# Performance work log

Hardware: AMD Instinct MI355X
Metric: run time of the kernel (lower is better)

## Reference

```python
import jax, jax.numpy as jnp
import numpy as np

LN_EPS = 1e-5

def setup_inputs() -> dict:
    key = jax.random.key(0)
    B, S, D = 4, 2048, 1024
    ks = jax.random.split(key, 8)
    sc = 1.0 / np.sqrt(D)
    inp = {
        'x': jax.random.normal(ks[0], (B, S, D), jnp.float32),
        'Wq': jax.random.normal(ks[1], (D, D), jnp.float32) * sc,
        'bq': jnp.zeros((D,), jnp.float32),
        'Wk': jax.random.normal(ks[2], (D, D), jnp.float32) * sc,
        'bk': jnp.zeros((D,), jnp.float32),
        'Wv': jax.random.normal(ks[3], (D, D), jnp.float32) * sc,
        'bv': jnp.zeros((D,), jnp.float32),
        'Wo': jax.random.normal(ks[4], (D, D), jnp.float32) * sc,
        'bo': jnp.zeros((D,), jnp.float32),
        'Wg_val': jax.random.normal(ks[5], (D, D), jnp.float32) * sc,
        'bg_val': jnp.zeros((D,), jnp.float32),
        'Wg_gate': jax.random.normal(ks[6], (D, D), jnp.float32) * sc,
        'bg_gate': jnp.zeros((D,), jnp.float32),
        'gamma': jnp.ones((D,), jnp.float32),
        'beta': jnp.zeros((D,), jnp.float32),
    }
    return inp


def reference(x, Wq, bq, Wk, bk, Wv, bv, Wo, bo, Wg_val, bg_val, Wg_gate, bg_gate, gamma, beta):
    # x: [B,S,D]
    q = jnp.einsum('bsd,de->bse', x, Wq) + bq
    k = jnp.einsum('bsd,de->bse', x, Wk) + bk
    v = jnp.einsum('bsd,de->bse', x, Wv) + bv
    scale = 1.0 / jnp.sqrt(jnp.asarray(q.shape[-1], q.dtype))
    qk = jnp.einsum('bqe,bke->bqk', q, k) * scale  # [B,S,S]
    a = jax.nn.softmax(qk, axis=-1)
    out = jnp.einsum('bqk,bke->bqe', a, v)
    out = jnp.einsum('bse,ed->bsd', out, Wo) + bo
    # GLU residual on q, then LayerNorm
    glu = (jnp.einsum('bse,ed->bsd', q, Wg_val) + bg_val) * jax.nn.sigmoid(jnp.einsum('bse,ed->bsd', q, Wg_gate) + bg_gate)
    out = out + glu
    mu = jnp.mean(out, axis=-1, keepdims=True)
    var = jnp.var(out, axis=-1, keepdims=True)
    out = (out - mu) * jax.lax.rsqrt(var + LN_EPS) * gamma + beta
    return out
```

## Files before the change

### kernel.cpp

```cpp
#include <hip/hip_runtime.h>
#include <hip/hip_bf16.h>
#include <cstdint>


typedef __bf16 bf16x8 __attribute__((ext_vector_type(8)));
typedef __bf16 bf16x4 __attribute__((ext_vector_type(4)));
typedef float f32x4 __attribute__((ext_vector_type(4)));

#define SYNC() do { asm volatile("" ::: "memory"); __builtin_amdgcn_s_barrier(); asm volatile("" ::: "memory"); } while (0)
#define WAITV(n) asm volatile("s_waitcnt vmcnt(" #n ")" ::: "memory")

__device__ __forceinline__ void gload_lds16(const void* g, void* l) {
    __builtin_amdgcn_global_load_lds(
        (__attribute__((address_space(1))) void*)(uintptr_t)g,
        (__attribute__((address_space(3))) void*)(uintptr_t)l,
        16, 0, 0);
}

__device__ __forceinline__ float to_f32(float x) { return x; }
__device__ __forceinline__ float to_f32(__hip_bfloat16 x) { return __bfloat162float(x); }

template <int EPI, bool VTS>
__global__ __launch_bounds__(512, 1) void gemm256(
    const __hip_bfloat16* __restrict__ A1, int lda1,
    const __hip_bfloat16* __restrict__ A2, int lda2, int nsplit,
    const __hip_bfloat16* __restrict__ Bt,
    __hip_bfloat16* __restrict__ Cout, const float* __restrict__ bias, float scale,
    __hip_bfloat16* __restrict__ vt, int vtc0,
    int K, int ldb, int ldc,
    long strideA, long strideB, long strideC)
{
    __shared__ __align__(16) char smem[131072];

    const int b = blockIdx.z;
    const int tid = threadIdx.x;
    const int lane = tid & 63;
    const int wm = (tid >> 6) & 1;
    const int wn = (tid >> 6) >> 1;

    const bool sel2 = ((int)blockIdx.y * 256) >= nsplit;
    const __hip_bfloat16* A = sel2 ? A2 : A1;
    const int lda = sel2 ? lda2 : lda1;

    const __hip_bfloat16* gA = A + (long)b * strideA + (long)blockIdx.x * 256 * lda;
    const __hip_bfloat16* gB = Bt + (long)b * strideB + (long)blockIdx.y * 256 * ldb;

    const int r0 = tid >> 3;
    const int s0 = (tid & 7) ^ (r0 & 7);
    const int r1 = r0 + 64;
    const int s1 = (tid & 7) ^ (r1 & 7);

#define STAGE(buf, isB, half, kt)                                                        \
    do {                                                                                 \
        const __hip_bfloat16* g_ = (isB) ? gB : gA;                                      \
        const int ld_ = (isB) ? ldb : lda;                                               \
        char* l_ = smem + (buf) * 65536 + (isB) * 32768 + (half) * 16384;                \
        gload_lds16(g_ + (long)((half) * 128 + r0) * ld_ + (kt) * 64 + s0 * 8, l_ + tid * 16);        \
        gload_lds16(g_ + (long)((half) * 128 + r1) * ld_ + (kt) * 64 + s1 * 8, l_ + 8192 + tid * 16); \
    } while (0)

    const int fr = lane & 15;
    const int kg = lane >> 4;

#define LDA_(dst, buf, mh, mi, kk)                                                       \
    do {                                                                                 \
        const int lr_ = wm * 64 + (mi) * 16 + fr;                                        \
        const int sl_ = ((kk) * 4 + kg) ^ (lr_ & 7);                                     \
        dst = *(const bf16x8*)(smem + (buf) * 65536 + (mh) * 16384 + lr_ * 128 + sl_ * 16); \
    } while (0)
#define LDB_(dst, buf, nh, ni, kk)                                                       \
    do {                                                                                 \
        const int lr_ = wn * 32 + (ni) * 16 + fr;                                        \
        const int sl_ = ((kk) * 4 + kg) ^ (lr_ & 7);                                     \
        dst = *(const bf16x8*)(smem + (buf) * 65536 + 32768 + (nh) * 16384 + lr_ * 128 + sl_ * 16); \
    } while (0)

    f32x4 acc[2][2][4][2];
#pragma unroll
    for (int mh = 0; mh < 2; ++mh)
#pragma unroll
        for (int nh = 0; nh < 2; ++nh)
#pragma unroll
            for (int mi = 0; mi < 4; ++mi)
#pragma unroll
                for (int ni = 0; ni < 2; ++ni) acc[mh][nh][mi][ni] = {0.f, 0.f, 0.f, 0.f};

    bf16x8 av[4][2], bv[2][2];

#define MFMA_QUAD(mh, nh)                                                                \
    do {                                                                                 \
        __builtin_amdgcn_s_setprio(1);                                                   \
        _Pragma("unroll")                                                                \
        for (int mi = 0; mi < 4; ++mi)                                                   \
            _Pragma("unroll")                                                            \
            for (int ni = 0; ni < 2; ++ni)                                               \
                _Pragma("unroll")                                                        \
                for (int kk = 0; kk < 2; ++kk)                                           \
                    acc[mh][nh][mi][ni] = __builtin_amdgcn_mfma_f32_16x16x32_bf16(       \
                        av[mi][kk], bv[ni][kk], acc[mh][nh][mi][ni], 0, 0, 0);           \
        __builtin_amdgcn_s_setprio(0);                                                   \
    } while (0)

    const int NT = K >> 6;

    STAGE(0, 0, 0, 0);
    STAGE(0, 1, 0, 0);
    STAGE(0, 1, 1, 0);
    STAGE(0, 0, 1, 0);
    WAITV(4);
    SYNC();

    for (int t = 0; t < NT - 1; ++t) {
        const int c = t & 1;
#pragma unroll
        for (int mi = 0; mi < 4; ++mi) { LDA_(av[mi][0], c, 0, mi, 0); LDA_(av[mi][1], c, 0, mi, 1); }
#pragma unroll
        for (int ni = 0; ni < 2; ++ni) { LDB_(bv[ni][0], c, 0, ni, 0); LDB_(bv[ni][1], c, 0, ni, 1); }
        STAGE(c ^ 1, 0, 0, t + 1);
        MFMA_QUAD(0, 0);
        WAITV(4);
        SYNC();
#pragma unroll
        for (int ni = 0; ni < 2; ++ni) { LDB_(bv[ni][0], c, 1, ni, 0); LDB_(bv[ni][1], c, 1, ni, 1); }
        STAGE(c ^ 1, 1, 0, t + 1);
        MFMA_QUAD(0, 1);
        WAITV(4);
        SYNC();
#pragma unroll
        for (int mi = 0; mi < 4; ++mi) { LDA_(av[mi][0], c, 1, mi, 0); LDA_(av[mi][1], c, 1, mi, 1); }
        STAGE(c ^ 1, 1, 1, t + 1);
        MFMA_QUAD(1, 1);
        SYNC();
#pragma unroll
        for (int ni = 0; ni < 2; ++ni) { LDB_(bv[ni][0], c, 0, ni, 0); LDB_(bv[ni][1], c, 0, ni, 1); }
        STAGE(c ^ 1, 0, 1, t + 1);
        MFMA_QUAD(1, 0);
        WAITV(4);
        SYNC();
    }

    {
        const int c = (NT - 1) & 1;
#pragma unroll
        for (int mi = 0; mi < 4; ++mi) { LDA_(av[mi][0], c, 0, mi, 0); LDA_(av[mi][1], c, 0, mi, 1); }
#pragma unroll
        for (int ni = 0; ni < 2; ++ni) { LDB_(bv[ni][0], c, 0, ni, 0); LDB_(bv[ni][1], c, 0, ni, 1); }
        MFMA_QUAD(0, 0);
        WAITV(2);
        SYNC();
#pragma unroll
        for (int ni = 0; ni < 2; ++ni) { LDB_(bv[ni][0], c, 1, ni, 0); LDB_(bv[ni][1], c, 1, ni, 1); }
        MFMA_QUAD(0, 1);
        WAITV(0);
        SYNC();
#pragma unroll
        for (int mi = 0; mi < 4; ++mi) { LDA_(av[mi][0], c, 1, mi, 0); LDA_(av[mi][1], c, 1, mi, 1); }
        MFMA_QUAD(1, 1);
#pragma unroll
        for (int ni = 0; ni < 2; ++ni) { LDB_(bv[ni][0], c, 0, ni, 0); LDB_(bv[ni][1], c, 0, ni, 1); }
        MFMA_QUAD(1, 0);
    }

    const long row0 = (long)blockIdx.x * 256 + wm * 64 + (lane >> 4) * 4;
    const long col0 = (long)blockIdx.y * 256 + wn * 32 + (lane & 15);
#pragma unroll
    for (int mh = 0; mh < 2; ++mh) {
#pragma unroll
        for (int nh = 0; nh < 2; ++nh) {
#pragma unroll
            for (int ni = 0; ni < 2; ++ni) {
                const long col = col0 + nh * 128 + ni * 16;
                const float bval = (EPI == 0 && bias != nullptr) ? bias[col] : 0.f;
#pragma unroll
                for (int mi = 0; mi < 4; ++mi) {
                    const long row = row0 + mh * 128 + mi * 16;
                    if (VTS && col >= vtc0) {
                        const int b_ = (int)(row >> 11);
                        const int s_ = (int)(row & 2047);
                        bf16x4 pk;
#pragma unroll
                        for (int i = 0; i < 4; ++i) pk[i] = (__bf16)(acc[mh][nh][mi][ni][i] + bval);
                        *(bf16x4*)(vt + ((long)b_ << 21) + (long)(col - vtc0) * 2048 + s_) = pk;
                    } else {
#pragma unroll
                        for (int i = 0; i < 4; ++i) {
                            const float v = (EPI == 1) ? acc[mh][nh][mi][ni][i] * scale
                                                       : acc[mh][nh][mi][ni][i] + bval;
                            Cout[(long)b * strideC + (row + i) * (long)ldc + col] = __float2bfloat16(v);
                        }
                    }
                }
            }
        }
    }
#undef STAGE
#undef LDA_
#undef LDB_
#undef MFMA_QUAD
}

__global__ __launch_bounds__(512, 1) void gemm_tn128(
    const __hip_bfloat16* __restrict__ A, int lda,
    const __hip_bfloat16* __restrict__ Bt,
    __hip_bfloat16* __restrict__ Cout, const float* __restrict__ bias,
    int K, int ldb, int ldc,
    long strideA, long strideB, long strideC)
{
    __shared__ __align__(16) char smem[147456];

    const int b = blockIdx.z;
    const int tid = threadIdx.x;
    const int lane = tid & 63;
    const int wid = tid >> 6;
    const int wm = wid & 3;
    const int wn = wid >> 2;

    const __hip_bfloat16* gA = A + (long)b * strideA + (long)blockIdx.x * 256 * lda;
    const __hip_bfloat16* gB = Bt + (long)b * strideB + (long)blockIdx.y * 128 * ldb;

    const int r0 = tid >> 3, r1 = r0 + 64;
    const int s0 = (tid & 7) ^ (r0 & 7);
    const int s1 = (tid & 7) ^ (r1 & 7);

#define STG_A(base_, h_, kt_)                                                                              \
    do {                                                                                                   \
        gload_lds16(gA + (long)((h_) * 128 + r0) * lda + (kt_) * 64 + s0 * 8, (base_) + (h_) * 16384 + tid * 16);        \
        gload_lds16(gA + (long)((h_) * 128 + r1) * lda + (kt_) * 64 + s1 * 8, (base_) + (h_) * 16384 + 8192 + tid * 16); \
    } while (0)
#define STG_B(base_, kt_)                                                                                  \
    do {                                                                                                   \
        gload_lds16(gB + (long)r0 * ldb + (kt_) * 64 + s0 * 8, (base_) + 32768 + tid * 16);                \
        gload_lds16(gB + (long)r1 * ldb + (kt_) * 64 + s1 * 8, (base_) + 32768 + 8192 + tid * 16);         \
    } while (0)

    const int fr = lane & 15;
    const int kg = lane >> 4;

#define LD_A(dst, base_, mi_, kk_)                                                        \
    do {                                                                                  \
        const int row_ = wm * 64 + (mi_) * 16 + fr;                                       \
        const int sl_ = ((kk_) * 4 + kg) ^ (row_ & 7);                                    \
        dst = *(const bf16x8*)((base_) + row_ * 128 + sl_ * 16);                          \
    } while (0)
#define LD_B(dst, base_, ni_, kk_)                                                        \
    do {                                                                                  \
        const int row_ = wn * 64 + (ni_) * 16 + fr;                                       \
        const int sl_ = ((kk_) * 4 + kg) ^ (row_ & 7);                                    \
        dst = *(const bf16x8*)((base_) + 32768 + row_ * 128 + sl_ * 16);                  \
    } while (0)

    f32x4 acc[4][4];
#pragma unroll
    for (int mi = 0; mi < 4; ++mi)
#pragma unroll
        for (int ni = 0; ni < 4; ++ni) acc[mi][ni] = {0.f, 0.f, 0.f, 0.f};

    const int NT = K >> 6;

    STG_A(smem, 0, 0); STG_A(smem, 1, 0); STG_B(smem, 0);
    STG_A(smem + 49152, 0, 1); STG_A(smem + 49152, 1, 1); STG_B(smem + 49152, 1);
    WAITV(6);
    SYNC();

    int bi = 0;
    for (int t = 0; t < NT; ++t) {
        char* base = smem + bi * 49152;
        if (t + 2 < NT) {
            int bs = bi + 2; if (bs >= 3) bs -= 3;
            char* sb = smem + bs * 49152;
            STG_A(sb, 0, t + 2); STG_A(sb, 1, t + 2); STG_B(sb, t + 2);
        }
        bf16x8 av[4], bv[4];
#pragma unroll
        for (int kk = 0; kk < 2; ++kk) {
#pragma unroll
            for (int mi = 0; mi < 4; ++mi) LD_A(av[mi], base, mi, kk);
#pragma unroll
            for (int ni = 0; ni < 4; ++ni) LD_B(bv[ni], base, ni, kk);
            __builtin_amdgcn_s_setprio(1);
#pragma unroll
            for (int mi = 0; mi < 4; ++mi)
#pragma unroll
                for (int ni = 0; ni < 4; ++ni)
                    acc[mi][ni] = __builtin_amdgcn_mfma_f32_16x16x32_bf16(av[mi], bv[ni], acc[mi][ni], 0, 0, 0);
            __builtin_amdgcn_s_setprio(0);
        }
        if (t + 2 < NT) { WAITV(6); SYNC(); }
        else if (t + 1 < NT) { WAITV(0); SYNC(); }
        bi = (bi + 1 == 3) ? 0 : bi + 1;
    }

    const long row0 = (long)blockIdx.x * 256 + wm * 64 + (lane >> 4) * 4;
    const long col0 = (long)blockIdx.y * 128 + wn * 64 + (lane & 15);
#pragma unroll
    for (int ni = 0; ni < 4; ++ni) {
        const long col = col0 + ni * 16;
        const float bval = (bias != nullptr) ? bias[col] : 0.f;
#pragma unroll
        for (int mi = 0; mi < 4; ++mi) {
#pragma unroll
            for (int i = 0; i < 4; ++i) {
                const long row = row0 + mi * 16 + i;
                Cout[(long)b * strideC + row * (long)ldc + col] = __float2bfloat16(acc[mi][ni][i] + bval);
            }
        }
    }
#undef STG_A
#undef STG_B
#undef LD_A
#undef LD_B
}

__global__ __launch_bounds__(256) void transpose6(
    const float* __restrict__ W0, const float* __restrict__ W1, const float* __restrict__ W2,
    const float* __restrict__ W3, const float* __restrict__ W4, const float* __restrict__ W5,
    __hip_bfloat16* __restrict__ dst)
{
    __shared__ float tile[32][33];
    const int z = blockIdx.z;
    const float* pin = (z == 0) ? W0 : (z == 1) ? W1 : (z == 2) ? W2 : (z == 3) ? W3 : (z == 4) ? W4 : W5;
    __hip_bfloat16* pout = dst + (long)z * 1024 * 1024;
    const int tx = threadIdx.x, ty = threadIdx.y;
    const int c0 = blockIdx.x * 32, r0 = blockIdx.y * 32;
#pragma unroll
    for (int j = 0; j < 4; ++j)
        tile[ty + j * 8][tx] = pin[(long)(r0 + ty + j * 8) * 1024 + c0 + tx];
    __syncthreads();
#pragma unroll
    for (int j = 0; j < 4; ++j)
        pout[(long)(c0 + ty + j * 8) * 1024 + r0 + tx] = __float2bfloat16(tile[tx][ty + j * 8]);
}

__global__ __launch_bounds__(256) void f32_to_bf16_vec(
    const float* __restrict__ in, __hip_bfloat16* __restrict__ out, long n4)
{
    const long i = (long)blockIdx.x * 256 + threadIdx.x;
    if (i >= n4) return;
    const float4 v = ((const float4*)in)[i];
    union { __hip_bfloat16 h[4]; ushort4 u; } cv;
    cv.h[0] = __float2bfloat16(v.x);
    cv.h[1] = __float2bfloat16(v.y);
    cv.h[2] = __float2bfloat16(v.z);
    cv.h[3] = __float2bfloat16(v.w);
    ((ushort4*)out)[i] = cv.u;
}

__global__ __launch_bounds__(256) void concat_bias(
    const float* __restrict__ bq, const float* __restrict__ bk, const float* __restrict__ bv,
    const float* __restrict__ bo, const float* __restrict__ bgv, const float* __restrict__ bgg,
    float* __restrict__ out)
{
    const int i = blockIdx.x * 256 + threadIdx.x;
    float v;
    if (i < 1024) v = bq[i];
    else if (i < 2048) v = bk[i - 1024];
    else if (i < 3072) v = bv[i - 2048];
    else if (i < 4096) v = bo[i - 3072];
    else if (i < 5120) v = bgv[i - 4096];
    else v = bgg[i - 5120];
    out[i] = v;
}

__global__ __launch_bounds__(256) void softmax_kernel(
    const __hip_bfloat16* __restrict__ S, __hip_bfloat16* __restrict__ P)
{
    const long row = blockIdx.x;
    const __hip_bfloat16* s = S + row * 2048;
    __hip_bfloat16* p = P + row * 2048;
    const int t = threadIdx.x;
    const bf16x8 v8 = *(const bf16x8*)(s + t * 8);
    float v[8];
    float mx = -1e30f;
#pragma unroll
    for (int j = 0; j < 8; ++j) { v[j] = (float)v8[j]; mx = fmaxf(mx, v[j]); }
#pragma unroll
    for (int off = 32; off; off >>= 1) mx = fmaxf(mx, __shfl_xor(mx, off));
    __shared__ float wred[4];
    __shared__ float wsum[4];
    const int w = t >> 6;
    if ((t & 63) == 0) wred[w] = mx;
    __syncthreads();
    mx = fmaxf(fmaxf(wred[0], wred[1]), fmaxf(wred[2], wred[3]));
    float sum = 0.f;
#pragma unroll
    for (int j = 0; j < 8; ++j) { v[j] = __expf(v[j] - mx); sum += v[j]; }
#pragma unroll
    for (int off = 32; off; off >>= 1) sum += __shfl_xor(sum, off);
    if ((t & 63) == 0) wsum[w] = sum;
    __syncthreads();
    sum = wsum[0] + wsum[1] + wsum[2] + wsum[3];
    const float inv = 1.0f / sum;
    bf16x8 o8;
#pragma unroll
    for (int j = 0; j < 8; ++j) o8[j] = (__bf16)(v[j] * inv);
    *(bf16x8*)(p + t * 8) = o8;
}

__global__ __launch_bounds__(256) void glu_ln_kernel(
    const __hip_bfloat16* __restrict__ T1G,
    const float* __restrict__ gamma, const float* __restrict__ beta, float* __restrict__ out)
{
    const long row = blockIdx.x;
    const __hip_bfloat16* pr = T1G + row * 3072;
    const int t = threadIdx.x;
    const int c0 = t * 4;
    const bf16x4 t1 = *(const bf16x4*)(pr + c0);
    const bf16x4 gv = *(const bf16x4*)(pr + 1024 + c0);
    const bf16x4 gg = *(const bf16x4*)(pr + 2048 + c0);
    float y[4];
    float s = 0.f, ss = 0.f;
#pragma unroll
    for (int j = 0; j < 4; ++j) {
        const float g = (float)gv[j] * (1.0f / (1.0f + __expf(-(float)gg[j])));
        const float val = (float)t1[j] + g;
        y[j] = val; s += val; ss += val * val;
    }
#pragma unroll
    for (int off = 32; off; off >>= 1) { s += __shfl_xor(s, off); ss += __shfl_xor(ss, off); }
    __shared__ float rs[4], rss[4];
    const int w = t >> 6;
    if ((t & 63) == 0) { rs[w] = s; rss[w] = ss; }
    __syncthreads();
    s = rs[0] + rs[1] + rs[2] + rs[3];
    ss = rss[0] + rss[1] + rss[2] + rss[3];
    const float mu = s * (1.0f / 1024.0f);
    const float var = ss * (1.0f / 1024.0f) - mu * mu;
    const float r = rsqrtf(var + 1e-5f);
    const float4 gm = *(const float4*)(gamma + c0);
    const float4 bt = *(const float4*)(beta + c0);
    float4 o;
    o.x = (y[0] - mu) * r * gm.x + bt.x;
    o.y = (y[1] - mu) * r * gm.y + bt.y;
    o.z = (y[2] - mu) * r * gm.z + bt.z;
    o.w = (y[3] - mu) * r * gm.w + bt.w;
    *(float4*)(out + row * 1024 + c0) = o;
}

extern "C" void kernel_launch(void* const* d_in, const int* in_sizes, int n_in,
                              void* d_out, int out_size, void* d_ws, size_t ws_size,
                              hipStream_t stream)
{
    const int B = 4, S = 2048, D = 1024;
    const float* x    = (const float*)d_in[0];
    const float* Wq   = (const float*)d_in[1];
    const float* bq   = (const float*)d_in[2];
    const float* Wk   = (const float*)d_in[3];
    const float* bk   = (const float*)d_in[4];
    const float* Wv   = (const float*)d_in[5];
    const float* bv   = (const float*)d_in[6];
    const float* Wo   = (const float*)d_in[7];
    const float* bo   = (const float*)d_in[8];
    const float* Wgv  = (const float*)d_in[9];
    const float* bgv  = (const float*)d_in[10];
    const float* Wgg  = (const float*)d_in[11];
    const float* bgg  = (const float*)d_in[12];
    const float* gamma = (const float*)d_in[13];
    const float* beta  = (const float*)d_in[14];
    float* out = (float*)d_out;

    char* ws = (char*)d_ws;
    size_t off = 0;
    auto take = [&](size_t bytes) { char* p = ws + off; off += (bytes + 255) & ~(size_t)255; return p; };

    __hip_bfloat16* wcat   = (__hip_bfloat16*)take((size_t)6 * D * D * 2);
    float*          bcat   = (float*)take((size_t)6 * D * 4);
    __hip_bfloat16* xb     = (__hip_bfloat16*)take((size_t)B * S * D * 2);
    __hip_bfloat16* QKVb   = (__hip_bfloat16*)take((size_t)B * S * 3 * D * 2);
    __hip_bfloat16* Vtb    = (__hip_bfloat16*)take((size_t)B * S * D * 2);
    __hip_bfloat16* scoresb = (__hip_bfloat16*)take((size_t)B * S * S * 2);
    __hip_bfloat16* Pb     = (__hip_bfloat16*)take((size_t)B * S * S * 2);
    __hip_bfloat16* Oatt   = (__hip_bfloat16*)take((size_t)B * S * D * 2);
    __hip_bfloat16* T1G    = (__hip_bfloat16*)take((size_t)B * S * 3 * D * 2);

    const long SD = (long)S * D, SS = (long)S * S, S3D = (long)S * 3 * D;
    const float att_scale = 0.03125f;
    const __hip_bfloat16* Qb = QKVb;
    const __hip_bfloat16* Kb = QKVb + D;

    f32_to_bf16_vec<<<dim3((unsigned)((long)B * S * D / 4 / 256)), dim3(256), 0, stream>>>(x, xb, (long)B * S * D / 4);
    transpose6<<<dim3(D / 32, D / 32, 6), dim3(32, 8), 0, stream>>>(Wq, Wk, Wv, Wo, Wgv, Wgg, wcat);
    concat_bias<<<dim3(24), dim3(256), 0, stream>>>(bq, bk, bv, bo, bgv, bgg, bcat);

    gemm256<0, true><<<dim3(B * S / 256, 3 * D / 256, 1), dim3(512), 0, stream>>>(
        xb, D, xb, D, 1 << 30, wcat, QKVb, bcat, 1.f, Vtb, 2 * D,
        D, D, 3 * D, 0, 0, 0);

    gemm256<1, false><<<dim3(S / 256, S / 256, B), dim3(512), 0, stream>>>(
        Qb, 3 * D, Qb, 3 * D, 1 << 30, Kb, scoresb, nullptr, att_scale, nullptr, 1 << 30,
        D, 3 * D, S, S3D, S3D, SS);

    softmax_kernel<<<dim3(B * S), dim3(256), 0, stream>>>(scoresb, Pb);

    gemm_tn128<<<dim3(S / 256, D / 128, B), dim3(512), 0, stream>>>(
        Pb, S, Vtb, Oatt, nullptr, S, S, D, SS, SD, SD);

    gemm256<0, false><<<dim3(B * S / 256, 3 * D / 256, 1), dim3(512), 0, stream>>>(
        Oatt, D, QKVb, 3 * D, D, wcat + (size_t)3 * D * D, T1G, bcat + 3 * D, 1.f, nullptr, 1 << 30,
        D, D, 3 * D, 0, 0, 0);

    glu_ln_kernel<<<dim3(B * S), dim3(256), 0, stream>>>(T1G, gamma, beta, out);
}
```

Baseline: 244.6 us.

## Split fused QKV and output GEMMs into separate QK and V/gate launches

The fused QKV projection is split in two: a 256x256 GEMM writes Q and K, and a separate 128-wide-tile GEMM writes V directly in transposed layout. The final fused output GEMM is also split, with the gate projection moved to the 128-wide kernel. This shrinks the grid of the 256-tile kernels, presumably to fix wave quantization across the CUs and to take the transposed-store branch out of the big GEMM's epilogue. The cost is two extra kernel launches and re-reading xb and Q in separate passes.

```diff
diff --git a/kernel.cpp b/kernel.cpp
--- a/kernel.cpp
+++ b/kernel.cpp
@@ -17,16 +17,12 @@
         16, 0, 0);
 }
 
-__device__ __forceinline__ float to_f32(float x) { return x; }
-__device__ __forceinline__ float to_f32(__hip_bfloat16 x) { return __bfloat162float(x); }
-
-template <int EPI, bool VTS>
+template <int EPI>
 __global__ __launch_bounds__(512, 1) void gemm256(
     const __hip_bfloat16* __restrict__ A1, int lda1,
     const __hip_bfloat16* __restrict__ A2, int lda2, int nsplit,
     const __hip_bfloat16* __restrict__ Bt,
     __hip_bfloat16* __restrict__ Cout, const float* __restrict__ bias, float scale,
-    __hip_bfloat16* __restrict__ vt, int vtc0,
     int K, int ldb, int ldc,
     long strideA, long strideB, long strideC)
 {
@@ -174,20 +170,11 @@
 #pragma unroll
                 for (int mi = 0; mi < 4; ++mi) {
                     const long row = row0 + mh * 128 + mi * 16;
-                    if (VTS && col >= vtc0) {
-                        const int b_ = (int)(row >> 11);
-                        const int s_ = (int)(row & 2047);
-                        bf16x4 pk;
-#pragma unroll
-                        for (int i = 0; i < 4; ++i) pk[i] = (__bf16)(acc[mh][nh][mi][ni][i] + bval);
-                        *(bf16x4*)(vt + ((long)b_ << 21) + (long)(col - vtc0) * 2048 + s_) = pk;
-                    } else {
-#pragma unroll
-                        for (int i = 0; i < 4; ++i) {
-                            const float v = (EPI == 1) ? acc[mh][nh][mi][ni][i] * scale
-                                                       : acc[mh][nh][mi][ni][i] + bval;
-                            Cout[(long)b * strideC + (row + i) * (long)ldc + col] = __float2bfloat16(v);
-                        }
+#pragma unroll
+                    for (int i = 0; i < 4; ++i) {
+                        const float v = (EPI == 1) ? acc[mh][nh][mi][ni][i] * scale
+                                                   : acc[mh][nh][mi][ni][i] + bval;
+                        Cout[(long)b * strideC + (row + i) * (long)ldc + col] = __float2bfloat16(v);
                     }
                 }
             }
@@ -199,10 +186,12 @@
 #undef MFMA_QUAD
 }
 
+template <int VTS>
 __global__ __launch_bounds__(512, 1) void gemm_tn128(
     const __hip_bfloat16* __restrict__ A, int lda,
     const __hip_bfloat16* __restrict__ Bt,
     __hip_bfloat16* __restrict__ Cout, const float* __restrict__ bias,
+    __hip_bfloat16* __restrict__ vt,
     int K, int ldb, int ldc,
     long strideA, long strideB, long strideC)
 {
@@ -298,10 +287,18 @@
         const float bval = (bias != nullptr) ? bias[col] : 0.f;
 #pragma unroll
         for (int mi = 0; mi < 4; ++mi) {
-#pragma unroll
-            for (int i = 0; i < 4; ++i) {
-                const long row = row0 + mi * 16 + i;
-                Cout[(long)b * strideC + row * (long)ldc + col] = __float2bfloat16(acc[mi][ni][i] + bval);
+            const long row = row0 + mi * 16;
+            if (VTS) {
+                const int b_ = (int)(row >> 11);
+                const int s_ = (int)(row & 2047);
+                bf16x4 pk;
+#pragma unroll
+                for (int i = 0; i < 4; ++i) pk[i] = (__bf16)(acc[mi][ni][i] + bval);
+                *(bf16x4*)(vt + ((long)b_ << 21) + col * 2048 + s_) = pk;
+            } else {
+#pragma unroll
+                for (int i = 0; i < 4; ++i)
+                    Cout[(long)b * strideC + (row + i) * (long)ldc + col] = __float2bfloat16(acc[mi][ni][i] + bval);
             }
         }
     }
@@ -465,37 +462,45 @@
     __hip_bfloat16* wcat   = (__hip_bfloat16*)take((size_t)6 * D * D * 2);
     float*          bcat   = (float*)take((size_t)6 * D * 4);
     __hip_bfloat16* xb     = (__hip_bfloat16*)take((size_t)B * S * D * 2);
-    __hip_bfloat16* QKVb   = (__hip_bfloat16*)take((size_t)B * S * 3 * D * 2);
+    __hip_bfloat16* QKb    = (__hip_bfloat16*)take((size_t)B * S * 2 * D * 2);
     __hip_bfloat16* Vtb    = (__hip_bfloat16*)take((size_t)B * S * D * 2);
     __hip_bfloat16* scoresb = (__hip_bfloat16*)take((size_t)B * S * S * 2);
     __hip_bfloat16* Pb     = (__hip_bfloat16*)take((size_t)B * S * S * 2);
     __hip_bfloat16* Oatt   = (__hip_bfloat16*)take((size_t)B * S * D * 2);
     __hip_bfloat16* T1G    = (__hip_bfloat16*)take((size_t)B * S * 3 * D * 2);
 
-    const long SD = (long)S * D, SS = (long)S * S, S3D = (long)S * 3 * D;
+    const long SD = (long)S * D, SS = (long)S * S, S2D = (long)S * 2 * D;
     const float att_scale = 0.03125f;
-    const __hip_bfloat16* Qb = QKVb;
-    const __hip_bfloat16* Kb = QKVb + D;
+    const __hip_bfloat16* Qb = QKb;
+    const __hip_bfloat16* Kb = QKb + D;
 
     f32_to_bf16_vec<<<dim3((unsigned)((long)B * S * D / 4 / 256)), dim3(256), 0, stream>>>(x, xb, (long)B * S * D / 4);
     transpose6<<<dim3(D / 32, D / 32, 6), dim3(32, 8), 0, stream>>>(Wq, Wk, Wv, Wo, Wgv, Wgg, wcat);
     concat_bias<<<dim3(24), dim3(256), 0, stream>>>(bq, bk, bv, bo, bgv, bgg, bcat);
 
-    gemm256<0, true><<<dim3(B * S / 256, 3 * D / 256, 1), dim3(512), 0, stream>>>(
-        xb, D, xb, D, 1 << 30, wcat, QKVb, bcat, 1.f, Vtb, 2 * D,
+    gemm256<0><<<dim3(B * S / 256, 2 * D / 256, 1), dim3(512), 0, stream>>>(
+        xb, D, xb, D, 1 << 30, wcat, QKb, bcat, 1.f,
+        D, D, 2 * D, 0, 0, 0);
+
+    gemm_tn128<1><<<dim3(B * S / 256, D / 128, 1), dim3(512), 0, stream>>>(
+        xb, D, wcat + (size_t)2 * D * D, nullptr, bcat + 2 * D, Vtb,
+        D, D, 0, 0, 0, 0);
+
+    gemm256<1><<<dim3(S / 256, S / 256, B), dim3(512), 0, stream>>>(
+        Qb, 2 * D, Qb, 2 * D, 1 << 30, Kb, scoresb, nullptr, att_scale,
+        D, 2 * D, S, S2D, S2D, SS);
+
+    softmax_kernel<<<dim3(B * S), dim3(256), 0, stream>>>(scoresb, Pb);
+
+    gemm_tn128<0><<<dim3(S / 256, D / 128, B), dim3(512), 0, stream>>>(
+        Pb, S, Vtb, Oatt, nullptr, nullptr, S, S, D, SS, SD, SD);
+
+    gemm256<0><<<dim3(B * S / 256, 2 * D / 256, 1), dim3(512), 0, stream>>>(
+        Oatt, D, QKb, 2 * D, D, wcat + (size_t)3 * D * D, T1G, bcat + 3 * D, 1.f,
         D, D, 3 * D, 0, 0, 0);
 
-    gemm256<1, false><<<dim3(S / 256, S / 256, B), dim3(512), 0, stream>>>(
-        Qb, 3 * D, Qb, 3 * D, 1 << 30, Kb, scoresb, nullptr, att_scale, nullptr, 1 << 30,
-        D, 3 * D, S, S3D, S3D, SS);
-
-    softmax_kernel<<<dim3(B * S), dim3(256), 0, stream>>>(scoresb, Pb);
-
-    gemm_tn128<<<dim3(S / 256, D / 128, B), dim3(512), 0, stream>>>(
-        Pb, S, Vtb, Oatt, nullptr, S, S, D, SS, SD, SD);
-
-    gemm256<0, false><<<dim3(B * S / 256, 3 * D / 256, 1), dim3(512), 0, stream>>>(
-        Oatt, D, QKVb, 3 * D, D, wcat + (size_t)3 * D * D, T1G, bcat + 3 * D, 1.f, nullptr, 1 << 30,
+    gemm_tn128<0><<<dim3(B * S / 256, D / 128, 1), dim3(512), 0, stream>>>(
+        QKb, 2 * D, wcat + (size_t)5 * D * D, T1G + 2 * D, bcat + 5 * D, nullptr,
         D, D, 3 * D, 0, 0, 0);
 
     glu_ln_kernel<<<dim3(B * S), dim3(256), 0, stream>>>(T1G, gamma, beta, out);
```

After: 240.8 us. No clear change (-1.6%).
